# Performance work log

Hardware: AMD Instinct MI355X
Metric: run time of the kernel (lower is better)

Reference implementation:

```python
import jax, jax.numpy as jnp
import numpy as np

DIM = 256; HEADS = 8; DEPTH = 2; DFF = 128
T = 64      # timesteps (transformer batch dim for s_transformer)
N = 2048    # total agents
S = 256     # number of segments (scenes)
L = 8       # agents per segment (N = S*L)
HD = DIM // HEADS
LN_EPS = 1e-5


def _ln(x, w, b):
    m = x.mean(-1, keepdims=True)
    v = x.var(-1, keepdims=True)
    return (x - m) / jnp.sqrt(v + LN_EPS) * w + b


def _mha(x, qkvw, qkvb, ow, ob):
    B, Sq, D = x.shape
    qkv = x @ qkvw.T + qkvb                      # [B,Sq,3D]
    q, k, v = jnp.split(qkv, 3, axis=-1)
    def sp(t):
        return t.reshape(B, Sq, HEADS, HD).transpose(0, 2, 1, 3)
    q, k, v = sp(q), sp(k), sp(v)
    a = jax.nn.softmax(jnp.einsum('bhqd,bhkd->bhqk', q, k) * (1.0 / (HD ** 0.5)))
    o = jnp.einsum('bhqk,bhkd->bhqd', a, v).transpose(0, 2, 1, 3).reshape(B, Sq, D)
    return o @ ow.T + ob


def _layer(x, qkvw, qkvb, ow, ob, l1w, l1b, l2w, l2b, ln1w, ln1b, ln2w, ln2b):
    # PyTorch TransformerEncoderLayer, post-norm, relu FFN
    x = _ln(x + _mha(x, qkvw, qkvb, ow, ob), ln1w, ln1b)
    h = jax.nn.relu(x @ l1w.T + l1b) @ l2w.T + l2b
    return _ln(x + h, ln2w, ln2b)


def _encoder(x, qkvw, qkvb, ow, ob, l1w, l1b, l2w, l2b, ln1w, ln1b, ln2w, ln2b):
    for i in range(DEPTH):
        x = _layer(x, qkvw[i], qkvb[i], ow[i], ob[i], l1w[i], l1b[i],
                   l2w[i], l2b[i], ln1w[i], ln1b[i], ln2w[i], ln2b[i])
    return x


def setup_inputs() -> dict:
    key = jax.random.key(0)
    ks = iter(jax.random.split(key, 64))
    def rn(shape, scale=0.05):
        return jax.random.normal(next(ks), shape, dtype=jnp.float32) * scale
    inp = {}
    inp['moveinfo'] = jax.random.normal(next(ks), (N, T, 2), dtype=jnp.float32)
    starts = jnp.arange(S, dtype=jnp.int32) * L
    inp['seq_start_end'] = jnp.stack([starts, starts + L], axis=1)  # [S,2]
    inp['w_in'] = rn((DIM, 2)); inp['b_in'] = rn((DIM,))
    for p in ('s', 't'):
        inp[p + '_qkvw'] = rn((DEPTH, 3 * DIM, DIM)); inp[p + '_qkvb'] = rn((DEPTH, 3 * DIM))
        inp[p + '_ow'] = rn((DEPTH, DIM, DIM)); inp[p + '_ob'] = rn((DEPTH, DIM))
        inp[p + '_l1w'] = rn((DEPTH, DFF, DIM)); inp[p + '_l1b'] = rn((DEPTH, DFF))
        inp[p + '_l2w'] = rn((DEPTH, DIM, DFF)); inp[p + '_l2b'] = rn((DEPTH, DIM))
        inp[p + '_ln1w'] = jnp.ones((DEPTH, DIM)); inp[p + '_ln1b'] = jnp.zeros((DEPTH, DIM))
        inp[p + '_ln2w'] = jnp.ones((DEPTH, DIM)); inp[p + '_ln2b'] = jnp.zeros((DEPTH, DIM))
    return inp


def reference(moveinfo, seq_start_end, w_in, b_in,
              s_qkvw, s_qkvb, s_ow, s_ob, s_l1w, s_l1b, s_l2w, s_l2b,
              s_ln1w, s_ln1b, s_ln2w, s_ln2b,
              t_qkvw, t_qkvb, t_ow, t_ob, t_l1w, t_l1b, t_l2w, t_l2b,
              t_ln1w, t_ln1b, t_ln2w, t_ln2b):
    # to_dim: Linear(2, dim) + exact GELU
    s_in = jax.nn.gelu(jnp.einsum('ntc,dc->ntd', moveinfo, w_in) + b_in, approximate=False)
    s_in = s_in.transpose(1, 0, 2)                       # [T, N, D]
    # gather equal-length segments: ragged loop batched as one attention call
    idx = seq_start_end[:, 0][:, None] + jnp.arange(L)   # [S, L]
    seg = s_in[:, idx, :].reshape(T * S, L, DIM)         # [T*S, L, D]
    cls = jnp.full((T * S, 1, DIM), 1e-5, dtype=s_in.dtype)
    x = jnp.concatenate([cls, seg], axis=1)              # [T*S, 1+L, D]
    x = _encoder(x, s_qkvw, s_qkvb, s_ow, s_ob, s_l1w, s_l1b, s_l2w, s_l2b,
                 s_ln1w, s_ln1b, s_ln2w, s_ln2b)
    t_in = x[:, 0, :].reshape(T, S, DIM).transpose(1, 0, 2)  # [S, T, D]
    out = _encoder(t_in, t_qkvw, t_qkvb, t_ow, t_ob, t_l1w, t_l1b, t_l2w, t_l2b,
                   t_ln1w, t_ln1b, t_ln2w, t_ln2b)
    return out
```

## Files before the change

### kernel.cpp

```cpp
#include <hip/hip_runtime.h>
#include <hip/hip_bf16.h>
#include <math.h>

typedef __bf16 bf16_t;
typedef float floatx4 __attribute__((ext_vector_type(4)));
typedef bf16_t bf16x8 __attribute__((ext_vector_type(8)));

typedef __attribute__((address_space(1))) void g_void;
typedef __attribute__((address_space(3))) void lds_void;

__device__ __forceinline__ void ldg_lds16(const bf16_t* g, bf16_t* l) {
    __builtin_amdgcn_global_load_lds((g_void*)g, (lds_void*)l, 16, 0, 0);
}

__device__ __forceinline__ void unpack4(uint2 r, float* o) {
    o[0] = __uint_as_float((r.x & 0xffffu) << 16); o[1] = __uint_as_float(r.x & 0xffff0000u);
    o[2] = __uint_as_float((r.y & 0xffffu) << 16); o[3] = __uint_as_float(r.y & 0xffff0000u);
}

__global__ void cvt_weights(const float* __restrict__ sqkvw, const float* __restrict__ sow,
                            const float* __restrict__ sl1w,  const float* __restrict__ sl2w,
                            const float* __restrict__ tqkvw, const float* __restrict__ tow,
                            const float* __restrict__ tl1w,  const float* __restrict__ tl2w,
                            bf16_t* __restrict__ dst) {
    int i = blockIdx.x * 256 + threadIdx.x;
    float v;
    if      (i <  393216) v = sqkvw[i];
    else if (i <  524288) v = sow  [i -  393216];
    else if (i <  589824) v = sl1w [i -  524288];
    else if (i <  655360) v = sl2w [i -  589824];
    else if (i < 1048576) v = tqkvw[i -  655360];
    else if (i < 1179648) v = tow  [i - 1048576];
    else if (i < 1245184) v = tl1w [i - 1179648];
    else                  v = tl2w [i - 1245184];
    dst[i] = (bf16_t)v;
}

__global__ void embed_k(const float* __restrict__ mv, const float* __restrict__ w_in,
                        const float* __restrict__ b_in, bf16_t* __restrict__ x, int b0) {
    int blk = blockIdx.x; int d = threadIdx.x;
    int tok = blk % 9; int lb = blk / 9;
    size_t oidx = (size_t)blk * 256 + d;
    if (tok == 0) { x[oidx] = (bf16_t)1e-5f; return; }
    int bb = b0 + lb; int t = bb >> 8; int s = bb & 255;
    int n = s * 8 + (tok - 1);
    float m0 = mv[((size_t)n * 64 + t) * 2];
    float m1 = mv[((size_t)n * 64 + t) * 2 + 1];
    float v = m0 * w_in[2 * d] + m1 * w_in[2 * d + 1] + b_in[d];
    v = 0.5f * v * (1.0f + erff(v * 0.70710678118654752f));
    x[oidx] = (bf16_t)v;
}

__global__ void cls_k(const bf16_t* __restrict__ x, bf16_t* __restrict__ txb,
                      float* __restrict__ txf, int b0) {
    int lb = blockIdx.x; int d = threadIdx.x;
    int bb = b0 + lb; int t = bb >> 8; int s = bb & 255;
    bf16_t v = x[(size_t)lb * 2304 + d];
    size_t di = ((size_t)(s * 64 + t)) * 256 + d;
    txb[di] = v;
    txf[di] = (float)v;
}

__global__ __launch_bounds__(256) void gemm_bt(const bf16_t* __restrict__ A,
                                               const bf16_t* __restrict__ W,
                                               const float* __restrict__ bias,
                                               bf16_t* __restrict__ C,
                                               int M, int N, int K, int relu) {
    __shared__ __align__(16) bf16_t As[8192];
    __shared__ __align__(16) bf16_t Ws[8192];
    int MT = M >> 7, NT = N >> 7;
    int g = blockIdx.x;
    int m_t, n_t;
    if ((MT & 7) == 0) {
        int x = g & 7, q = g >> 3;
        m_t = (q / NT) * 8 + x;
        n_t = q % NT;
    } else {
        m_t = g / NT; n_t = g % NT;
    }
    int tid = threadIdx.x;
    int lane = tid & 63;
    int wave = tid >> 6;
    int m0 = m_t * 128;
    int n0 = n_t * 128;
    int wm = (wave & 1) * 64;
    int wn = (wave >> 1) * 64;
    int fm = lane & 15;
    int fq = lane >> 4;

    floatx4 acc[4][4] = {};

    const bf16_t* Ag = A + (size_t)(m0 + (tid >> 2)) * K + (tid & 3) * 8;
    const bf16_t* Wg = W + (size_t)(n0 + (tid >> 2)) * K + (tid & 3) * 8;

    auto STAGE = [&](int r, int b) {
        int k = r * 32;
        ldg_lds16(Ag + k,                   &As[b * 4096 + tid * 8]);
        ldg_lds16(Ag + k + (size_t)64 * K,  &As[b * 4096 + 2048 + tid * 8]);
        ldg_lds16(Wg + k,                   &Ws[b * 4096 + tid * 8]);
        ldg_lds16(Wg + k + (size_t)64 * K,  &Ws[b * 4096 + 2048 + tid * 8]);
    };
    auto COMPUTE = [&](int b) {
        bf16x8 af[4], wf[4];
#pragma unroll
        for (int mi = 0; mi < 4; mi++)
            af[mi] = *(const bf16x8*)&As[b * 4096 + (wm + mi * 16 + fm) * 32 + fq * 8];
#pragma unroll
        for (int ni = 0; ni < 4; ni++)
            wf[ni] = *(const bf16x8*)&Ws[b * 4096 + (wn + ni * 16 + fm) * 32 + fq * 8];
#pragma unroll
        for (int mi = 0; mi < 4; mi++)
#pragma unroll
            for (int ni = 0; ni < 4; ni++)
                acc[mi][ni] = __builtin_amdgcn_mfma_f32_16x16x32_bf16(wf[ni], af[mi], acc[mi][ni], 0, 0, 0);
    };

    int nr = K >> 5;
    STAGE(0, 0);
    __syncthreads();
    for (int r = 0; r + 1 < nr; ++r) {
        STAGE(r + 1, (r + 1) & 1);
        COMPUTE(r & 1);
        __syncthreads();
    }
    COMPUTE((nr - 1) & 1);

#pragma unroll
    for (int mi = 0; mi < 4; mi++) {
        int row = m0 + wm + mi * 16 + fm;
#pragma unroll
        for (int ni = 0; ni < 4; ni++) {
            int colb = n0 + wn + ni * 16 + fq * 4;
            float4 b4 = *(const float4*)(bias + colb);
            float v0 = acc[mi][ni][0] + b4.x;
            float v1 = acc[mi][ni][1] + b4.y;
            float v2 = acc[mi][ni][2] + b4.z;
            float v3 = acc[mi][ni][3] + b4.w;
            if (relu) {
                v0 = fmaxf(v0, 0.f); v1 = fmaxf(v1, 0.f);
                v2 = fmaxf(v2, 0.f); v3 = fmaxf(v3, 0.f);
            }
            bf16_t t4[4] = {(bf16_t)v0, (bf16_t)v1, (bf16_t)v2, (bf16_t)v3};
            *(uint2*)(C + (size_t)row * N + colb) = *(uint2*)t4;
        }
    }
}

__device__ __forceinline__ void epi_resln64(
    floatx4 (&acc)[4][4], int m0, int wn, int fm, int fq, int wave,
    const float* __restrict__ bias, const bf16_t* __restrict__ res_bf,
    const float* __restrict__ res_f, const float* __restrict__ lnw,
    const float* __restrict__ lnb, bf16_t* __restrict__ out_bf,
    float* __restrict__ out_f, float (*rs)[64], float (*rss)[64]) {
    float s[4] = {0.f, 0.f, 0.f, 0.f}, ss[4] = {0.f, 0.f, 0.f, 0.f};
#pragma unroll
    for (int mi = 0; mi < 4; mi++) {
        size_t row = (size_t)(m0 + mi * 16 + fm);
#pragma unroll
        for (int ni = 0; ni < 4; ni++) {
            int col = wn + ni * 16 + fq * 4;
            float4 b4 = *(const float4*)(bias + col);
            float r4[4];
            if (res_f) {
                float4 t = *(const float4*)(res_f + row * 256 + col);
                r4[0] = t.x; r4[1] = t.y; r4[2] = t.z; r4[3] = t.w;
            } else {
                unpack4(*(const uint2*)(res_bf + row * 256 + col), r4);
            }
            float v0 = acc[mi][ni][0] + b4.x + r4[0];
            float v1 = acc[mi][ni][1] + b4.y + r4[1];
            float v2 = acc[mi][ni][2] + b4.z + r4[2];
            float v3 = acc[mi][ni][3] + b4.w + r4[3];
            acc[mi][ni][0] = v0; acc[mi][ni][1] = v1;
            acc[mi][ni][2] = v2; acc[mi][ni][3] = v3;
            s[mi] += v0 + v1 + v2 + v3;
            ss[mi] += v0 * v0 + v1 * v1 + v2 * v2 + v3 * v3;
        }
    }
#pragma unroll
    for (int mi = 0; mi < 4; mi++) {
        s[mi]  += __shfl_xor(s[mi], 16);  s[mi]  += __shfl_xor(s[mi], 32);
        ss[mi] += __shfl_xor(ss[mi], 16); ss[mi] += __shfl_xor(ss[mi], 32);
    }
    if (fq == 0) {
#pragma unroll
        for (int mi = 0; mi < 4; mi++) {
            rs [wave][mi * 16 + fm] = s[mi];
            rss[wave][mi * 16 + fm] = ss[mi];
        }
    }
    __syncthreads();
#pragma unroll
    for (int mi = 0; mi < 4; mi++) {
        int lrow = mi * 16 + fm;
        size_t row = (size_t)(m0 + lrow);
        float mean = (rs[0][lrow] + rs[1][lrow] + rs[2][lrow] + rs[3][lrow]) * (1.f / 256.f);
        float var  = (rss[0][lrow] + rss[1][lrow] + rss[2][lrow] + rss[3][lrow]) * (1.f / 256.f)
                   - mean * mean;
        float inv = rsqrtf(var + 1e-5f);
#pragma unroll
        for (int ni = 0; ni < 4; ni++) {
            int col = wn + ni * 16 + fq * 4;
            float4 w4 = *(const float4*)(lnw + col);
            float4 bl = *(const float4*)(lnb + col);
            float o0 = (acc[mi][ni][0] - mean) * inv * w4.x + bl.x;
            float o1 = (acc[mi][ni][1] - mean) * inv * w4.y + bl.y;
            float o2 = (acc[mi][ni][2] - mean) * inv * w4.z + bl.z;
            float o3 = (acc[mi][ni][3] - mean) * inv * w4.w + bl.w;
            if (out_bf) {
                bf16_t t4[4] = {(bf16_t)o0, (bf16_t)o1, (bf16_t)o2, (bf16_t)o3};
                *(uint2*)(out_bf + row * 256 + col) = *(uint2*)t4;
            }
            if (out_f) {
                float4 t; t.x = o0; t.y = o1; t.z = o2; t.w = o3;
                *(float4*)(out_f + row * 256 + col) = t;
            }
        }
    }
}

__global__ __launch_bounds__(256) void gemm_proj_ln(const bf16_t* __restrict__ A,
                                                    const bf16_t* __restrict__ W,
                                                    const float* __restrict__ bias,
                                                    const bf16_t* __restrict__ res_bf,
                                                    const float* __restrict__ res_f,
                                                    const float* __restrict__ lnw,
                                                    const float* __restrict__ lnb,
                                                    bf16_t* __restrict__ out_bf,
                                                    float* __restrict__ out_f) {
    __shared__ __align__(16) bf16_t As[4096];
    __shared__ __align__(16) bf16_t Ws[16384];
    __shared__ float rs[4][64], rss[4][64];
    int tid = threadIdx.x;
    int lane = tid & 63, wave = tid >> 6;
    int m0 = blockIdx.x * 64;
    int wn = wave * 64;
    int fm = lane & 15, fq = lane >> 4;
    floatx4 acc[4][4] = {};
    const bf16_t* Ag = A + (size_t)(m0 + (tid >> 2)) * 256 + (tid & 3) * 8;
    const bf16_t* Wg = W + (size_t)(tid >> 2) * 256 + (tid & 3) * 8;

    auto STAGE = [&](int r, int b) {
        int k = r * 32;
        ldg_lds16(Ag + k, &As[b * 2048 + tid * 8]);
#pragma unroll
        for (int j = 0; j < 4; j++)
            ldg_lds16(Wg + k + j * 16384, &Ws[b * 8192 + j * 2048 + tid * 8]);
    };
    auto COMPUTE = [&](int b) {
        bf16x8 af[4], wf[4];
#pragma unroll
        for (int mi = 0; mi < 4; mi++)
            af[mi] = *(const bf16x8*)&As[b * 2048 + (mi * 16 + fm) * 32 + fq * 8];
#pragma unroll
        for (int ni = 0; ni < 4; ni++)
            wf[ni] = *(const bf16x8*)&Ws[b * 8192 + (wn + ni * 16 + fm) * 32 + fq * 8];
#pragma unroll
        for (int mi = 0; mi < 4; mi++)
#pragma unroll
            for (int ni = 0; ni < 4; ni++)
                acc[mi][ni] = __builtin_amdgcn_mfma_f32_16x16x32_bf16(wf[ni], af[mi], acc[mi][ni], 0, 0, 0);
    };

    STAGE(0, 0);
    __syncthreads();
    for (int r = 0; r < 7; ++r) {
        STAGE(r + 1, (r + 1) & 1);
        COMPUTE(r & 1);
        __syncthreads();
    }
    COMPUTE(1);
    epi_resln64(acc, m0, wn, fm, fq, wave, bias, res_bf, res_f, lnw, lnb, out_bf, out_f, rs, rss);
}

__global__ __launch_bounds__(256) void gemm_ffn_ln(const bf16_t* __restrict__ X,
                                                   const bf16_t* __restrict__ w1,
                                                   const float* __restrict__ b1,
                                                   const bf16_t* __restrict__ w2,
                                                   const float* __restrict__ b2,
                                                   const float* __restrict__ lnw,
                                                   const float* __restrict__ lnb,
                                                   const float* __restrict__ res_f,
                                                   bf16_t* __restrict__ out_bf,
                                                   float* __restrict__ out_f) {
    __shared__ __align__(16) bf16_t As[4096];
    __shared__ __align__(16) bf16_t Ws[8192];
    __shared__ __align__(16) bf16_t Hs[10240];
    __shared__ float rs[4][64], rss[4][64];
    int tid = threadIdx.x, lane = tid & 63, wave = tid >> 6;
    int m0 = blockIdx.x * 64;
    int wn1 = wave * 32;
    int wn2 = wave * 64;
    int fm = lane & 15, fq = lane >> 4;
    floatx4 acc[4][2] = {};
    const bf16_t* Ag = X + (size_t)(m0 + (tid >> 2)) * 256 + (tid & 3) * 8;
    const bf16_t* Wg = w1 + (size_t)(tid >> 2) * 256 + (tid & 3) * 8;

    auto STAGE = [&](int r, int b) {
        int k = r * 32;
        ldg_lds16(Ag + k, &As[b * 2048 + tid * 8]);
#pragma unroll
        for (int j = 0; j < 2; j++)
            ldg_lds16(Wg + k + j * 16384, &Ws[b * 4096 + j * 2048 + tid * 8]);
    };
    auto COMPUTE = [&](int b) {
        bf16x8 af[4], wf[2];
#pragma unroll
        for (int mi = 0; mi < 4; mi++)
            af[mi] = *(const bf16x8*)&As[b * 2048 + (mi * 16 + fm) * 32 + fq * 8];
#pragma unroll
        for (int ni = 0; ni < 2; ni++)
            wf[ni] = *(const bf16x8*)&Ws[b * 4096 + (wn1 + ni * 16 + fm) * 32 + fq * 8];
#pragma unroll
        for (int mi = 0; mi < 4; mi++)
#pragma unroll
            for (int ni = 0; ni < 2; ni++)
                acc[mi][ni] = __builtin_amdgcn_mfma_f32_16x16x32_bf16(wf[ni], af[mi], acc[mi][ni], 0, 0, 0);
    };

    STAGE(0, 0);
    __syncthreads();
    for (int r = 0; r < 7; ++r) {
        STAGE(r + 1, (r + 1) & 1);
        COMPUTE(r & 1);
        __syncthreads();
    }
    COMPUTE(1);

#pragma unroll
    for (int mi = 0; mi < 4; mi++) {
        int row = mi * 16 + fm;
#pragma unroll
        for (int ni = 0; ni < 2; ni++) {
            int c = wn1 + ni * 16 + fq * 4;
            float4 b4 = *(const float4*)(b1 + c);
            bf16_t t4[4];
            t4[0] = (bf16_t)fmaxf(acc[mi][ni][0] + b4.x, 0.f);
            t4[1] = (bf16_t)fmaxf(acc[mi][ni][1] + b4.y, 0.f);
            t4[2] = (bf16_t)fmaxf(acc[mi][ni][2] + b4.z, 0.f);
            t4[3] = (bf16_t)fmaxf(acc[mi][ni][3] + b4.w, 0.f);
            *(uint2*)&Hs[(c >> 5) * 2560 + row * 40 + (c & 31)] = *(uint2*)t4;
        }
    }
    __syncthreads();
    floatx4 acc2[4][4] = {};
#pragma unroll
    for (int ks = 0; ks < 4; ks++) {
        bf16x8 af2[4];
#pragma unroll
        for (int mi = 0; mi < 4; mi++)
            af2[mi] = *(const bf16x8*)&Hs[ks * 2560 + (mi * 16 + fm) * 40 + fq * 8];
#pragma unroll
        for (int ni = 0; ni < 4; ni++) {
            bf16x8 wf2 = *(const bf16x8*)(w2 + (size_t)(wn2 + ni * 16 + fm) * 128 + ks * 32 + fq * 8);
#pragma unroll
            for (int mi = 0; mi < 4; mi++)
                acc2[mi][ni] = __builtin_amdgcn_mfma_f32_16x16x32_bf16(wf2, af2[mi], acc2[mi][ni], 0, 0, 0);
        }
    }
    epi_resln64(acc2, m0, wn2, fm, fq, wave, b2, X, res_f, lnw, lnb, out_bf, out_f, rs, rss);
}

__global__ __launch_bounds__(256) void attn9_k(const bf16_t* __restrict__ qkv,
                                               bf16_t* __restrict__ ao) {
    __shared__ __align__(16) bf16_t sb[27648];
    int b = blockIdx.x; int tid = threadIdx.x;
    const uint4* src = (const uint4*)(qkv + (size_t)b * 27648);
    uint4* dstl = (uint4*)sb;
    for (int c = tid; c < 3456; c += 256) dstl[c] = src[c];
    __syncthreads();
    for (int p = tid; p < 288; p += 256) {
        int s = p / 72; int rem = p - s * 72; int h = rem / 9; int i = rem - h * 9;
        const bf16_t* B = sb + s * 6912;
        const bf16_t* qp = B + i * 768 + h * 32;
        float qf[32];
#pragma unroll
        for (int c = 0; c < 4; c++) {
            bf16x8 t8 = *(const bf16x8*)(qp + c * 8);
#pragma unroll
            for (int e = 0; e < 8; e++) qf[c * 8 + e] = (float)t8[e];
        }
        float sc[9]; float mx = -1e30f;
#pragma unroll
        for (int j = 0; j < 9; j++) {
            const bf16_t* kp = B + j * 768 + 256 + h * 32;
            float d = 0.f;
#pragma unroll
            for (int c = 0; c < 4; c++) {
                bf16x8 t8 = *(const bf16x8*)(kp + c * 8);
#pragma unroll
                for (int e = 0; e < 8; e++) d += qf[c * 8 + e] * (float)t8[e];
            }
            d *= 0.17677669529663687f;
            sc[j] = d; mx = fmaxf(mx, d);
        }
        float den = 0.f;
#pragma unroll
        for (int j = 0; j < 9; j++) { sc[j] = __expf(sc[j] - mx); den += sc[j]; }
        float inv = 1.0f / den;
        float of[32] = {};
#pragma unroll
        for (int j = 0; j < 9; j++) {
            const bf16_t* vp = B + j * 768 + 512 + h * 32;
            float w = sc[j];
#pragma unroll
            for (int c = 0; c < 4; c++) {
                bf16x8 t8 = *(const bf16x8*)(vp + c * 8);
#pragma unroll
                for (int e = 0; e < 8; e++) of[c * 8 + e] += w * (float)t8[e];
            }
        }
        bf16_t* dst = ao + ((size_t)(b * 4 + s) * 9 + i) * 256 + h * 32;
#pragma unroll
        for (int c = 0; c < 4; c++) {
            bf16x8 o8;
#pragma unroll
            for (int e = 0; e < 8; e++) o8[e] = (bf16_t)(of[c * 8 + e] * inv);
            *(bf16x8*)(dst + c * 8) = o8;
        }
    }
}

__global__ __launch_bounds__(256) void attn64_k(const bf16_t* __restrict__ qkv,
                                                bf16_t* __restrict__ ao) {
    __shared__ __align__(16) float kk[64 * 36];
    __shared__ __align__(16) float vv[64 * 36];
    __shared__ __align__(16) float pp[64 * 64];
    __shared__ float mloc[4 * 64];
    __shared__ float sloc[4 * 64];
    int s = blockIdx.x >> 3, h = blockIdx.x & 7;
    int t = threadIdx.x;
    int i = t & 63;
    int wq = t >> 6;

    {
        int r = t >> 2, c = t & 3;
        const bf16_t* kb = qkv + ((size_t)(s * 64 + r)) * 768 + h * 32 + 256 + c * 8;
        bf16x8 k8 = *(const bf16x8*)kb;
        bf16x8 v8 = *(const bf16x8*)(kb + 256);
        float* kd = &kk[r * 36 + c * 8];
        float* vd = &vv[r * 36 + c * 8];
#pragma unroll
        for (int e = 0; e < 8; e++) { kd[e] = (float)k8[e]; vd[e] = (float)v8[e]; }
    }
    const bf16_t* qb = qkv + ((size_t)(s * 64 + i)) * 768 + h * 32;
    float qf[32];
#pragma unroll
    for (int c = 0; c < 4; c++) {
        bf16x8 t8 = *(const bf16x8*)(qb + c * 8);
#pragma unroll
        for (int e = 0; e < 8; e++) qf[c * 8 + e] = (float)t8[e];
    }
    __syncthreads();

    float sc[16]; float mx = -1e30f;
#pragma unroll
    for (int jj = 0; jj < 16; jj++) {
        int j = wq * 16 + jj;
        const float* kr = &kk[j * 36];
        float d = 0.f;
#pragma unroll
        for (int c = 0; c < 8; c++) {
            float4 k4 = *(const float4*)(kr + c * 4);
            d += qf[c*4+0]*k4.x + qf[c*4+1]*k4.y + qf[c*4+2]*k4.z + qf[c*4+3]*k4.w;
        }
        d *= 0.17677669529663687f;
        sc[jj] = d; mx = fmaxf(mx, d);
    }
    float se = 0.f;
#pragma unroll
    for (int jj = 0; jj < 16; jj++) se += __expf(sc[jj] - mx);
    mloc[wq * 64 + i] = mx;
    sloc[wq * 64 + i] = se;
    __syncthreads();

    float m0 = mloc[i], m1 = mloc[64 + i], m2 = mloc[128 + i], m3 = mloc[192 + i];
    float gm = fmaxf(fmaxf(m0, m1), fmaxf(m2, m3));
    float D = sloc[i] * __expf(m0 - gm) + sloc[64 + i] * __expf(m1 - gm)
            + sloc[128 + i] * __expf(m2 - gm) + sloc[192 + i] * __expf(m3 - gm);

#pragma unroll
    for (int jj = 0; jj < 16; jj++)
        pp[(wq * 16 + jj) * 64 + i] = __expf(sc[jj] - gm);
    __syncthreads();

    float of[8] = {};
    for (int j = 0; j < 64; j++) {
        float w = pp[j * 64 + i];
        const float* vr = &vv[j * 36 + wq * 8];
        float4 va = *(const float4*)vr;
        float4 vb = *(const float4*)(vr + 4);
        of[0] += w * va.x; of[1] += w * va.y; of[2] += w * va.z; of[3] += w * va.w;
        of[4] += w * vb.x; of[5] += w * vb.y; of[6] += w * vb.z; of[7] += w * vb.w;
    }
    float invD = 1.0f / D;
    bf16_t o8[8];
#pragma unroll
    for (int e = 0; e < 8; e++) o8[e] = (bf16_t)(of[e] * invD);
    *(uint4*)(ao + ((size_t)(s * 64 + i)) * 256 + h * 32 + wq * 8) = *(uint4*)o8;
}

extern "C" void kernel_launch(void* const* d_in, const int* in_sizes, int n_in,
                              void* d_out, int out_size, void* d_ws, size_t ws_size,
                              hipStream_t stream) {
    const float* mv   = (const float*)d_in[0];
    const float* w_in = (const float*)d_in[2];
    const float* b_in = (const float*)d_in[3];
    const float* sp[12]; const float* tp[12];
    for (int i = 0; i < 12; i++) { sp[i] = (const float*)d_in[4 + i]; tp[i] = (const float*)d_in[16 + i]; }

    bf16_t* wbf = (bf16_t*)d_ws;
    bf16_t* txb = wbf + 1310720;
    float*  txf = (float*)(txb + 4194304);
    bf16_t* pool = (bf16_t*)(txf + 4194304);

    long long headB = 2621440LL + 8388608LL + 16777216LL;
    long long cand[5] = {16384, 8192, 4096, 2048, 1024};
    int BC = 1024;
    for (int c = 0; c < 5; c++) {
        long long poolB = cand[c] * 11520LL * 2;
        if (poolB < 33554432LL) poolB = 33554432LL;
        if ((size_t)(headB + poolB) <= ws_size) { BC = (int)cand[c]; break; }
    }

    cvt_weights<<<5120, 256, 0, stream>>>(sp[0], sp[2], sp[4], sp[6], tp[0], tp[2], tp[4], tp[6], wbf);

    const int M = BC * 9;
    const int MT64 = M / 64;
    bf16_t* xc    = pool;
    bf16_t* qkvb_ = pool + (long long)BC * 2304;
    bf16_t* aob   = qkvb_ + (long long)BC * 6912;

    for (int b0 = 0; b0 < 16384; b0 += BC) {
        embed_k<<<dim3(M), 256, 0, stream>>>(mv, w_in, b_in, xc, b0);
        for (int l = 0; l < 2; l++) {
            const bf16_t* wq = wbf + 0      + l * 196608;
            const bf16_t* wo = wbf + 393216 + l * 65536;
            const bf16_t* w1 = wbf + 524288 + l * 32768;
            const bf16_t* w2 = wbf + 589824 + l * 32768;
            gemm_bt<<<dim3((M / 128) * 6), 256, 0, stream>>>(xc, wq, sp[1] + l * 768, qkvb_, M, 768, 256, 0);
            attn9_k<<<dim3(BC / 4), 256, 0, stream>>>(qkvb_, aob);
            gemm_proj_ln<<<dim3(MT64), 256, 0, stream>>>(aob, wo, sp[3] + l * 256,
                                                         xc, (const float*)nullptr,
                                                         sp[8] + l * 256, sp[9] + l * 256,
                                                         xc, (float*)nullptr);
            gemm_ffn_ln<<<dim3(MT64), 256, 0, stream>>>(xc, w1, sp[5] + l * 128,
                                                        w2, sp[7] + l * 256,
                                                        sp[10] + l * 256, sp[11] + l * 256,
                                                        (const float*)nullptr,
                                                        xc, (float*)nullptr);
        }
        cls_k<<<dim3(BC), 256, 0, stream>>>(xc, txb, txf, b0);
    }

    bf16_t* tqkv = pool;
    bf16_t* tao  = pool + 12582912;
    for (int l = 0; l < 2; l++) {
        gemm_bt<<<dim3(128 * 6), 256, 0, stream>>>(txb, wbf + 655360 + l * 196608, tp[1] + l * 768,
                                                   tqkv, 16384, 768, 256, 0);
        attn64_k<<<dim3(2048), 256, 0, stream>>>(tqkv, tao);
        gemm_proj_ln<<<dim3(256), 256, 0, stream>>>(tao, wbf + 1048576 + l * 65536, tp[3] + l * 256,
                                                    (const bf16_t*)nullptr, txf,
                                                    tp[8] + l * 256, tp[9] + l * 256,
                                                    txb, txf);
        gemm_ffn_ln<<<dim3(256), 256, 0, stream>>>(txb, wbf + 1179648 + l * 32768, tp[5] + l * 128,
                                                   wbf + 1245184 + l * 32768, tp[7] + l * 256,
                                                   tp[10] + l * 256, tp[11] + l * 256,
                                                   txf,
                                                   (l == 0) ? txb : (bf16_t*)nullptr,
                                                   (l == 0) ? txf : (float*)d_out);
    }
}
```

Before: 1.122 ms.

## Use fragment-major LDS layout, K=64 stages, and vmcnt-based pipelining in GEMMs

The GEMM kernels now stage tiles into LDS in MFMA-fragment-major order, so each lane's 16-byte read is contiguous and free of bank conflicts. The generic GEMM doubles its K step to 64 per stage, which halves the number of barriers. All three kernels replace __syncthreads with explicit s_waitcnt vmcnt(n) plus s_barrier, so the next stage's async global-to-LDS loads stay in flight while the current stage computes. This uses more LDS in gemm_bt and depends on vmcnt counts that must exactly match the number of issued loads.

```diff
diff --git a/kernel.cpp b/kernel.cpp
--- a/kernel.cpp
+++ b/kernel.cpp
@@ -17,6 +17,9 @@
     o[0] = __uint_as_float((r.x & 0xffffu) << 16); o[1] = __uint_as_float(r.x & 0xffff0000u);
     o[2] = __uint_as_float((r.y & 0xffffu) << 16); o[3] = __uint_as_float(r.y & 0xffff0000u);
 }
+
+#define VMCNT(n) asm volatile("s_waitcnt vmcnt(" #n ")" ::: "memory")
+#define BAR()    asm volatile("s_barrier" ::: "memory")
 
 __global__ void cvt_weights(const float* __restrict__ sqkvw, const float* __restrict__ sow,
                             const float* __restrict__ sl1w,  const float* __restrict__ sl2w,
@@ -66,8 +69,8 @@
                                                const float* __restrict__ bias,
                                                bf16_t* __restrict__ C,
                                                int M, int N, int K, int relu) {
-    __shared__ __align__(16) bf16_t As[8192];
-    __shared__ __align__(16) bf16_t Ws[8192];
+    __shared__ __align__(16) bf16_t As[16384];
+    __shared__ __align__(16) bf16_t Ws[16384];
     int MT = M >> 7, NT = N >> 7;
     int g = blockIdx.x;
     int m_t, n_t;
@@ -90,40 +93,47 @@
 
     floatx4 acc[4][4] = {};
 
-    const bf16_t* Ag = A + (size_t)(m0 + (tid >> 2)) * K + (tid & 3) * 8;
-    const bf16_t* Wg = W + (size_t)(n0 + (tid >> 2)) * K + (tid & 3) * 8;
-
     auto STAGE = [&](int r, int b) {
-        int k = r * 32;
-        ldg_lds16(Ag + k,                   &As[b * 4096 + tid * 8]);
-        ldg_lds16(Ag + k + (size_t)64 * K,  &As[b * 4096 + 2048 + tid * 8]);
-        ldg_lds16(Wg + k,                   &Ws[b * 4096 + tid * 8]);
-        ldg_lds16(Wg + k + (size_t)64 * K,  &Ws[b * 4096 + 2048 + tid * 8]);
+        int k0 = r * 64;
+#pragma unroll
+        for (int s = 0; s < 2; s++) {
+#pragma unroll
+            for (int i = 0; i < 2; i++) {
+                int f = wave * 2 + i;
+                ldg_lds16(A + (size_t)(m0 + f * 16 + fm) * K + k0 + s * 32 + fq * 8,
+                          &As[b * 8192 + s * 4096 + f * 512 + lane * 8]);
+                ldg_lds16(W + (size_t)(n0 + f * 16 + fm) * K + k0 + s * 32 + fq * 8,
+                          &Ws[b * 8192 + s * 4096 + f * 512 + lane * 8]);
+            }
+        }
     };
     auto COMPUTE = [&](int b) {
-        bf16x8 af[4], wf[4];
-#pragma unroll
-        for (int mi = 0; mi < 4; mi++)
-            af[mi] = *(const bf16x8*)&As[b * 4096 + (wm + mi * 16 + fm) * 32 + fq * 8];
-#pragma unroll
-        for (int ni = 0; ni < 4; ni++)
-            wf[ni] = *(const bf16x8*)&Ws[b * 4096 + (wn + ni * 16 + fm) * 32 + fq * 8];
-#pragma unroll
-        for (int mi = 0; mi < 4; mi++)
+#pragma unroll
+        for (int s = 0; s < 2; s++) {
+            bf16x8 af[4], wf[4];
+#pragma unroll
+            for (int mi = 0; mi < 4; mi++)
+                af[mi] = *(const bf16x8*)&As[b * 8192 + s * 4096 + ((wave & 1) * 4 + mi) * 512 + lane * 8];
 #pragma unroll
             for (int ni = 0; ni < 4; ni++)
-                acc[mi][ni] = __builtin_amdgcn_mfma_f32_16x16x32_bf16(wf[ni], af[mi], acc[mi][ni], 0, 0, 0);
+                wf[ni] = *(const bf16x8*)&Ws[b * 8192 + s * 4096 + ((wave >> 1) * 4 + ni) * 512 + lane * 8];
+#pragma unroll
+            for (int mi = 0; mi < 4; mi++)
+#pragma unroll
+                for (int ni = 0; ni < 4; ni++)
+                    acc[mi][ni] = __builtin_amdgcn_mfma_f32_16x16x32_bf16(wf[ni], af[mi], acc[mi][ni], 0, 0, 0);
+        }
     };
 
-    int nr = K >> 5;
+    int nr = K >> 6;
     STAGE(0, 0);
-    __syncthreads();
-    for (int r = 0; r + 1 < nr; ++r) {
-        STAGE(r + 1, (r + 1) & 1);
+    for (int r = 0; r < nr; ++r) {
+        if (r + 1 < nr) { STAGE(r + 1, (r + 1) & 1); VMCNT(8); }
+        else            { VMCNT(0); }
+        BAR();
         COMPUTE(r & 1);
-        __syncthreads();
-    }
-    COMPUTE((nr - 1) & 1);
+        BAR();
+    }
 
 #pragma unroll
     for (int mi = 0; mi < 4; mi++) {
@@ -237,24 +247,26 @@
     int wn = wave * 64;
     int fm = lane & 15, fq = lane >> 4;
     floatx4 acc[4][4] = {};
-    const bf16_t* Ag = A + (size_t)(m0 + (tid >> 2)) * 256 + (tid & 3) * 8;
-    const bf16_t* Wg = W + (size_t)(tid >> 2) * 256 + (tid & 3) * 8;
 
     auto STAGE = [&](int r, int b) {
-        int k = r * 32;
-        ldg_lds16(Ag + k, &As[b * 2048 + tid * 8]);
-#pragma unroll
-        for (int j = 0; j < 4; j++)
-            ldg_lds16(Wg + k + j * 16384, &Ws[b * 8192 + j * 2048 + tid * 8]);
+        int k0 = r * 32;
+        ldg_lds16(A + (size_t)(m0 + wave * 16 + fm) * 256 + k0 + fq * 8,
+                  &As[b * 2048 + wave * 512 + lane * 8]);
+#pragma unroll
+        for (int j = 0; j < 4; j++) {
+            int f = wave * 4 + j;
+            ldg_lds16(W + (size_t)(f * 16 + fm) * 256 + k0 + fq * 8,
+                      &Ws[b * 8192 + f * 512 + lane * 8]);
+        }
     };
     auto COMPUTE = [&](int b) {
         bf16x8 af[4], wf[4];
 #pragma unroll
         for (int mi = 0; mi < 4; mi++)
-            af[mi] = *(const bf16x8*)&As[b * 2048 + (mi * 16 + fm) * 32 + fq * 8];
+            af[mi] = *(const bf16x8*)&As[b * 2048 + mi * 512 + lane * 8];
 #pragma unroll
         for (int ni = 0; ni < 4; ni++)
-            wf[ni] = *(const bf16x8*)&Ws[b * 8192 + (wn + ni * 16 + fm) * 32 + fq * 8];
+            wf[ni] = *(const bf16x8*)&Ws[b * 8192 + (wave * 4 + ni) * 512 + lane * 8];
 #pragma unroll
         for (int mi = 0; mi < 4; mi++)
 #pragma unroll
@@ -263,13 +275,13 @@
     };
 
     STAGE(0, 0);
-    __syncthreads();
-    for (int r = 0; r < 7; ++r) {
-        STAGE(r + 1, (r + 1) & 1);
+    for (int r = 0; r < 8; ++r) {
+        if (r < 7) { STAGE(r + 1, (r + 1) & 1); VMCNT(5); }
+        else       { VMCNT(0); }
+        BAR();
         COMPUTE(r & 1);
-        __syncthreads();
-    }
-    COMPUTE(1);
+        BAR();
+    }
     epi_resln64(acc, m0, wn, fm, fq, wave, bias, res_bf, res_f, lnw, lnb, out_bf, out_f, rs, rss);
 }
 
@@ -293,24 +305,26 @@
     int wn2 = wave * 64;
     int fm = lane & 15, fq = lane >> 4;
     floatx4 acc[4][2] = {};
-    const bf16_t* Ag = X + (size_t)(m0 + (tid >> 2)) * 256 + (tid & 3) * 8;
-    const bf16_t* Wg = w1 + (size_t)(tid >> 2) * 256 + (tid & 3) * 8;
 
     auto STAGE = [&](int r, int b) {
-        int k = r * 32;
-        ldg_lds16(Ag + k, &As[b * 2048 + tid * 8]);
-#pragma unroll
-        for (int j = 0; j < 2; j++)
-            ldg_lds16(Wg + k + j * 16384, &Ws[b * 4096 + j * 2048 + tid * 8]);
+        int k0 = r * 32;
+        ldg_lds16(X + (size_t)(m0 + wave * 16 + fm) * 256 + k0 + fq * 8,
+                  &As[b * 2048 + wave * 512 + lane * 8]);
+#pragma unroll
+        for (int j = 0; j < 2; j++) {
+            int f = wave * 2 + j;
+            ldg_lds16(w1 + (size_t)(f * 16 + fm) * 256 + k0 + fq * 8,
+                      &Ws[b * 4096 + f * 512 + lane * 8]);
+        }
     };
     auto COMPUTE = [&](int b) {
         bf16x8 af[4], wf[2];
 #pragma unroll
         for (int mi = 0; mi < 4; mi++)
-            af[mi] = *(const bf16x8*)&As[b * 2048 + (mi * 16 + fm) * 32 + fq * 8];
+            af[mi] = *(const bf16x8*)&As[b * 2048 + mi * 512 + lane * 8];
 #pragma unroll
         for (int ni = 0; ni < 2; ni++)
-            wf[ni] = *(const bf16x8*)&Ws[b * 4096 + (wn1 + ni * 16 + fm) * 32 + fq * 8];
+            wf[ni] = *(const bf16x8*)&Ws[b * 4096 + (wave * 2 + ni) * 512 + lane * 8];
 #pragma unroll
         for (int mi = 0; mi < 4; mi++)
 #pragma unroll
@@ -319,13 +333,13 @@
     };
 
     STAGE(0, 0);
-    __syncthreads();
-    for (int r = 0; r < 7; ++r) {
-        STAGE(r + 1, (r + 1) & 1);
+    for (int r = 0; r < 8; ++r) {
+        if (r < 7) { STAGE(r + 1, (r + 1) & 1); VMCNT(3); }
+        else       { VMCNT(0); }
+        BAR();
         COMPUTE(r & 1);
-        __syncthreads();
-    }
-    COMPUTE(1);
+        BAR();
+    }
 
 #pragma unroll
     for (int mi = 0; mi < 4; mi++) {
```

Result: slower. 1.286 ms (+14.6%).

## Replace double-buffered K loop with single-buffered 64-wide K step in GEMM

Applied to the files above, without the earlier changes.

The GEMM main loop no longer prefetches the next 32-wide K slice into a second LDS buffer while computing the current one. It now loads a full 64-wide K chunk into the same LDS space, synchronizes, then runs two MFMA sub-steps, with two barriers per iteration. This halves the loop trip count and barrier frequency per K element, but removes the overlap of global-to-LDS loads with compute.

```diff
diff --git a/kernel.cpp b/kernel.cpp
--- a/kernel.cpp
+++ b/kernel.cpp
@@ -85,45 +85,45 @@
     int n0 = n_t * 128;
     int wm = (wave & 1) * 64;
     int wn = (wave >> 1) * 64;
+    int arow = tid >> 2;
+    int acol = (tid & 3) * 8;
     int fm = lane & 15;
     int fq = lane >> 4;
 
     floatx4 acc[4][4] = {};
 
-    const bf16_t* Ag = A + (size_t)(m0 + (tid >> 2)) * K + (tid & 3) * 8;
-    const bf16_t* Wg = W + (size_t)(n0 + (tid >> 2)) * K + (tid & 3) * 8;
-
-    auto STAGE = [&](int r, int b) {
-        int k = r * 32;
-        ldg_lds16(Ag + k,                   &As[b * 4096 + tid * 8]);
-        ldg_lds16(Ag + k + (size_t)64 * K,  &As[b * 4096 + 2048 + tid * 8]);
-        ldg_lds16(Wg + k,                   &Ws[b * 4096 + tid * 8]);
-        ldg_lds16(Wg + k + (size_t)64 * K,  &Ws[b * 4096 + 2048 + tid * 8]);
-    };
-    auto COMPUTE = [&](int b) {
-        bf16x8 af[4], wf[4];
-#pragma unroll
-        for (int mi = 0; mi < 4; mi++)
-            af[mi] = *(const bf16x8*)&As[b * 4096 + (wm + mi * 16 + fm) * 32 + fq * 8];
-#pragma unroll
-        for (int ni = 0; ni < 4; ni++)
-            wf[ni] = *(const bf16x8*)&Ws[b * 4096 + (wn + ni * 16 + fm) * 32 + fq * 8];
-#pragma unroll
-        for (int mi = 0; mi < 4; mi++)
+    const bf16_t* Ag = A + (size_t)(m0 + arow) * K + acol;
+    const bf16_t* Wg = W + (size_t)(n0 + arow) * K + acol;
+
+    for (int k0 = 0; k0 < K; k0 += 64) {
+        __syncthreads();
+        ldg_lds16(Ag + k0,                       &As[tid * 8]);
+        ldg_lds16(Ag + k0 + (size_t)64 * K,      &As[2048 + tid * 8]);
+        ldg_lds16(Ag + k0 + 32,                  &As[4096 + tid * 8]);
+        ldg_lds16(Ag + k0 + 32 + (size_t)64 * K, &As[6144 + tid * 8]);
+        ldg_lds16(Wg + k0,                       &Ws[tid * 8]);
+        ldg_lds16(Wg + k0 + (size_t)64 * K,      &Ws[2048 + tid * 8]);
+        ldg_lds16(Wg + k0 + 32,                  &Ws[4096 + tid * 8]);
+        ldg_lds16(Wg + k0 + 32 + (size_t)64 * K, &Ws[6144 + tid * 8]);
+        __syncthreads();
+
+#pragma unroll
+        for (int sl = 0; sl < 2; sl++) {
+            int base = sl * 4096;
+            bf16x8 af[4], wf[4];
+#pragma unroll
+            for (int mi = 0; mi < 4; mi++)
+                af[mi] = *(const bf16x8*)&As[base + (wm + mi * 16 + fm) * 32 + fq * 8];
 #pragma unroll
             for (int ni = 0; ni < 4; ni++)
-                acc[mi][ni] = __builtin_amdgcn_mfma_f32_16x16x32_bf16(wf[ni], af[mi], acc[mi][ni], 0, 0, 0);
-    };
-
-    int nr = K >> 5;
-    STAGE(0, 0);
-    __syncthreads();
-    for (int r = 0; r + 1 < nr; ++r) {
-        STAGE(r + 1, (r + 1) & 1);
-        COMPUTE(r & 1);
-        __syncthreads();
-    }
-    COMPUTE((nr - 1) & 1);
+                wf[ni] = *(const bf16x8*)&Ws[base + (wn + ni * 16 + fm) * 32 + fq * 8];
+#pragma unroll
+            for (int mi = 0; mi < 4; mi++)
+#pragma unroll
+                for (int ni = 0; ni < 4; ni++)
+                    acc[mi][ni] = __builtin_amdgcn_mfma_f32_16x16x32_bf16(wf[ni], af[mi], acc[mi][ni], 0, 0, 0);
+        }
+    }
 
 #pragma unroll
     for (int mi = 0; mi < 4; mi++) {
```

After: 1.106 ms. About the same (-1.4%).
